# Optimization experiments

Hardware: AMD Instinct MI355X
Metric: run time of the kernel (lower is better)

The kernel has to match this reference:

```python
import jax, jax.numpy as jnp
import numpy as np

NUM_CLASSES = 6     # terrain classes 0..5
NUM_SUBJECTS = 16   # subject ids 0..15
MARGIN = 1.0
EPS = 1e-6          # torch pairwise_distance eps (added to the difference)


def setup_inputs() -> dict:
    key = jax.random.key(0)
    k1, k2, k3 = jax.random.split(key, 3)
    B, D = 131072, 256
    emb = jax.random.normal(k1, (B, D), dtype=jnp.float32)
    labels = jax.random.randint(k2, (B,), 0, NUM_CLASSES)
    sbj = jax.random.randint(k3, (B,), 0, NUM_SUBJECTS)
    return {"emb": emb, "labels": labels, "sbj": sbj}


def reference(emb, labels, sbj):
    """Within-subject hard-negative triplet loss.

    For every (subject s, class c) group with >=2 positives and >=1 negative
    (negatives = same subject, different class):
      anchor = first positive (in batch order), positive = second positive,
      negative = hardest (closest to anchor) same-subject other-class sample.
    Loss = mean over valid triplets of relu(d(a,p) - d(a,n) + margin), p=2.
    """
    B, D = emb.shape
    # flat grid of all (subject, class) pairs: P = NUM_SUBJECTS * NUM_CLASSES
    s_grid = jnp.repeat(jnp.arange(NUM_SUBJECTS), NUM_CLASSES)
    c_grid = jnp.tile(jnp.arange(NUM_CLASSES), NUM_SUBJECTS)

    def per_pair(s, c):
        m_pos = (sbj == s) & (labels == c)          # (B,)
        m_neg = (sbj == s) & (labels != c)          # (B,)
        cs = jnp.cumsum(m_pos)
        anchor_idx = jnp.argmax(m_pos & (cs == 1))  # first positive in batch order
        pos_idx = jnp.argmax(m_pos & (cs == 2))     # second positive
        valid = (jnp.sum(m_pos) >= 2) & (jnp.sum(m_neg) >= 1)
        return anchor_idx, pos_idx, m_neg, valid

    anchor_idx, pos_idx, m_neg, valid = jax.vmap(per_pair)(s_grid, c_grid)

    a = emb[anchor_idx]                              # (P, D)
    # squared L2 distance from each anchor to every sample (for mining only;
    # argmin of squared distance == argmin of distance, matching torch.cdist)
    d2 = (jnp.sum(a * a, axis=-1)[:, None]
          + jnp.sum(emb * emb, axis=-1)[None, :]
          - 2.0 * (a @ emb.T))                       # (P, B)
    d2 = jnp.where(m_neg, d2, jnp.inf)
    neg_idx = jnp.argmin(d2, axis=1)                 # (P,) hardest negative

    p = emb[pos_idx]                                 # (P, D)
    n = emb[neg_idx]                                 # (P, D)
    # torch TripletMarginLoss uses pairwise_distance: ||x1 - x2 + eps||_2
    d_ap = jnp.linalg.norm(a - p + EPS, axis=-1)
    d_an = jnp.linalg.norm(a - n + EPS, axis=-1)
    per_triplet = jnp.maximum(d_ap - d_an + MARGIN, 0.0)

    vf = valid.astype(emb.dtype)
    cnt = jnp.sum(vf)
    loss = jnp.sum(per_triplet * vf) / jnp.maximum(cnt, 1.0)
    return jnp.where(cnt > 0, loss, jnp.zeros((), emb.dtype))
```

## Files before the change

### kernel.cpp

```cpp
#include <hip/hip_runtime.h>

#define NUM_CLASSES 6
#define NUM_SUBJECTS 16
#define NUM_PAIRS (NUM_CLASSES * NUM_SUBJECTS)
#define MARGIN 1.0f
#define EPS 1e-6f
#define INF_I 0x7fffffff


__device__ __forceinline__ float wredsum(float v) {
#pragma unroll
    for (int m = 32; m >= 1; m >>= 1) v += __shfl_xor(v, m, 64);
    return v;
}

__device__ __forceinline__ unsigned int fkey(float f) {
    unsigned int b = __float_as_uint(f);
    return (b & 0x80000000u) ? ~b : (b | 0x80000000u);
}

__device__ __forceinline__ unsigned short f2bf(float f) {
    unsigned int u = __float_as_uint(f);
    unsigned int r = u + 0x7fffu + ((u >> 16) & 1u);
    return (unsigned short)(r >> 16);
}

__global__ void k_init(int* min1, int* min2, int* cntPos, int* cntSbj,
                       unsigned long long* best, float* a2) {
    int t = threadIdx.x;
    if (t < NUM_PAIRS) {
        min1[t] = INF_I;
        min2[t] = INF_I;
        cntPos[t] = 0;
        best[t] = ~0ull;
        a2[t] = 0.f;
    }
    if (t < NUM_SUBJECTS) cntSbj[t] = 0;
}

__global__ void k_stats(const int* __restrict__ labels, const int* __restrict__ sbj,
                        int* min1, int* min2, int* cntPos, int* cntSbj, int B) {
    __shared__ int l1[NUM_PAIRS], l2[NUM_PAIRS], lcp[NUM_PAIRS], lcs[NUM_SUBJECTS];
    for (int t = threadIdx.x; t < NUM_PAIRS; t += blockDim.x) { l1[t] = INF_I; l2[t] = INF_I; lcp[t] = 0; }
    if (threadIdx.x < NUM_SUBJECTS) lcs[threadIdx.x] = 0;
    __syncthreads();
    int i = blockIdx.x * blockDim.x + threadIdx.x;
    if (i < B) {
        int s = sbj[i], c = labels[i];
        int p = s * NUM_CLASSES + c;
        int o = atomicMin(&l1[p], i);
        atomicMin(&l2[p], max(o, i));
        atomicAdd(&lcp[p], 1);
        atomicAdd(&lcs[s], 1);
    }
    __syncthreads();
    for (int t = threadIdx.x; t < NUM_PAIRS; t += blockDim.x) {
        int m1 = l1[t];
        if (m1 != INF_I) {
            int o = atomicMin(&min1[t], m1);
            atomicMin(&min2[t], max(o, m1));
            if (l2[t] != INF_I) atomicMin(&min2[t], l2[t]);
            atomicAdd(&cntPos[t], lcp[t]);
        }
    }
    if (threadIdx.x < NUM_SUBJECTS && lcs[threadIdx.x]) atomicAdd(&cntSbj[threadIdx.x], lcs[threadIdx.x]);
}

__global__ void k_gather(const float4* __restrict__ emb4, const int* __restrict__ min1,
                         float4* anchors4, float* a2, int B) {
    int p = blockIdx.x;
    int lane = threadIdx.x;
    int idx = min1[p];
    if (idx < 0 || idx >= B) idx = 0;
    float4 v = emb4[(size_t)idx * 64 + lane];
    anchors4[(size_t)p * 64 + lane] = v;
    float t = v.x * v.x + v.y * v.y + v.z * v.z + v.w * v.w;
    t = wredsum(t);
    if (lane == 0) a2[p] = t;
}

__global__ __launch_bounds__(512, 2) void k_mine(const float4* __restrict__ emb4,
                                                 const int* __restrict__ labels,
                                                 const int* __restrict__ sbj,
                                                 const float4* __restrict__ anchors4,
                                                 const float* __restrict__ a2,
                                                 unsigned long long* gbest, int B) {
    __shared__ unsigned long long ancB64[NUM_SUBJECTS * 385];
    __shared__ float a2l[NUM_PAIRS];
    __shared__ unsigned long long lbest[NUM_PAIRS];

    for (int u = threadIdx.x; u < NUM_PAIRS * 64; u += blockDim.x) {
        int row = u >> 6;
        int grp = u & 63;
        float4 v = anchors4[u];
        unsigned int lo = (unsigned int)f2bf(v.x) | ((unsigned int)f2bf(v.y) << 16);
        unsigned int hi = (unsigned int)f2bf(v.z) | ((unsigned int)f2bf(v.w) << 16);
        int s = row / NUM_CLASSES, c = row - s * NUM_CLASSES;
        ancB64[s * 385 + c * 64 + grp] = (unsigned long long)lo | ((unsigned long long)hi << 32);
    }
    for (int t = threadIdx.x; t < NUM_PAIRS; t += blockDim.x) {
        a2l[t] = a2[t];
        lbest[t] = ~0ull;
    }
    __syncthreads();

    const int lane = threadIdx.x & 63;
    const int wv = (int)(threadIdx.x >> 6);
    const int wavesPerBlk = (int)(blockDim.x >> 6);
    const int waveGlob = (int)blockIdx.x * wavesPerBlk + wv;
    const int nwv = (int)gridDim.x * wavesPerBlk;
    const int nchunk = (B + 63) >> 6;

    for (int ch = waveGlob; ch < nchunk; ch += nwv) {
        int i = ch * 64 + lane;
        bool valid = i < B;
        int ic = valid ? i : (B - 1);
        int s = sbj[ic];
        int lbl = labels[ic];
        const float4* row = emb4 + (size_t)ic * 64;
        const unsigned long long* anc = ancB64 + s * 385;
        float e2 = 0.f, d0 = 0.f, d1 = 0.f, d2v = 0.f, d3 = 0.f, d4 = 0.f, d5 = 0.f;
#pragma unroll 4
        for (int k = 0; k < 64; ++k) {
            float4 v = row[k];
            e2 = fmaf(v.x, v.x, fmaf(v.y, v.y, fmaf(v.z, v.z, fmaf(v.w, v.w, e2))));
            unsigned long long A;
            unsigned int lo, hi;
            float a0, a1, a2f, a3;
#define DOT(C, ACC)                                                              \
            A = anc[(C) * 64 + k];                                               \
            lo = (unsigned int)A; hi = (unsigned int)(A >> 32);                  \
            a0 = __uint_as_float(lo << 16);                                      \
            a1 = __uint_as_float(lo & 0xffff0000u);                              \
            a2f = __uint_as_float(hi << 16);                                     \
            a3 = __uint_as_float(hi & 0xffff0000u);                              \
            ACC = fmaf(a0, v.x, fmaf(a1, v.y, fmaf(a2f, v.z, fmaf(a3, v.w, ACC))));
            DOT(0, d0) DOT(1, d1) DOT(2, d2v) DOT(3, d3) DOT(4, d4) DOT(5, d5)
#undef DOT
        }
        if (valid) {
            int pb = s * NUM_CLASSES;
            float dc[NUM_CLASSES] = {d0, d1, d2v, d3, d4, d5};
#pragma unroll
            for (int c = 0; c < NUM_CLASSES; ++c) {
                if (c != lbl) {
                    float dd = a2l[pb + c] + e2 - 2.f * dc[c];
                    unsigned long long pk =
                        ((unsigned long long)fkey(dd) << 32) | (unsigned int)i;
                    atomicMin(&lbest[pb + c], pk);
                }
            }
        }
    }
    __syncthreads();
    for (int t = threadIdx.x; t < NUM_PAIRS; t += blockDim.x) {
        unsigned long long v = lbest[t];
        if (v != ~0ull) {
            unsigned long long cur = gbest[t];
            if (v < cur) atomicMin(&gbest[t], v);
        }
    }
}

__global__ __launch_bounds__(1024) void k_finalize(const float4* __restrict__ emb4,
                                                   const int* __restrict__ min1,
                                                   const int* __restrict__ min2,
                                                   const int* __restrict__ cntPos,
                                                   const int* __restrict__ cntSbj,
                                                   const unsigned long long* __restrict__ best,
                                                   float* out, int B) {
    __shared__ float vals[NUM_PAIRS];
    __shared__ int vld[NUM_PAIRS];
    int wave = threadIdx.x >> 6;
    int lane = threadIdx.x & 63;
    for (int p = wave; p < NUM_PAIRS; p += (blockDim.x >> 6)) {
        int s = p / NUM_CLASSES;
        int ai = min1[p], pi = min2[p];
        int npos = cntPos[p];
        int nneg = cntSbj[s] - npos;
        unsigned long long bb = best[p];
        int ni = (int)(bb & 0xffffffffu);
        bool ok = (npos >= 2) && (nneg >= 1) && (bb != ~0ull);
        if (ai < 0 || ai >= B) ai = 0;
        if (pi < 0 || pi >= B) pi = 0;
        if (ni < 0 || ni >= B) ni = 0;
        float4 a = emb4[(size_t)ai * 64 + lane];
        float4 pp = emb4[(size_t)pi * 64 + lane];
        float4 nn = emb4[(size_t)ni * 64 + lane];
        float dap = 0.f, dan = 0.f, t;
        t = a.x - pp.x + EPS; dap += t * t;
        t = a.y - pp.y + EPS; dap += t * t;
        t = a.z - pp.z + EPS; dap += t * t;
        t = a.w - pp.w + EPS; dap += t * t;
        t = a.x - nn.x + EPS; dan += t * t;
        t = a.y - nn.y + EPS; dan += t * t;
        t = a.z - nn.z + EPS; dan += t * t;
        t = a.w - nn.w + EPS; dan += t * t;
        dap = wredsum(dap);
        dan = wredsum(dan);
        if (lane == 0) {
            float lv = sqrtf(dap) - sqrtf(dan) + MARGIN;
            vals[p] = ok ? fmaxf(lv, 0.f) : 0.f;
            vld[p] = ok ? 1 : 0;
        }
    }
    __syncthreads();
    if (threadIdx.x == 0) {
        float sum = 0.f;
        int cnt = 0;
        for (int p = 0; p < NUM_PAIRS; ++p) { sum += vals[p]; cnt += vld[p]; }
        out[0] = (cnt > 0) ? (sum / (float)cnt) : 0.f;
    }
}

extern "C" void kernel_launch(void* const* d_in, const int* in_sizes, int n_in,
                              void* d_out, int out_size, void* d_ws, size_t ws_size,
                              hipStream_t stream) {
    const float* emb = (const float*)d_in[0];
    const int* labels = (const int*)d_in[1];
    const int* sbj = (const int*)d_in[2];
    float* out = (float*)d_out;
    const int B = in_sizes[1];
    const float4* emb4 = (const float4*)emb;

    char* ws = (char*)d_ws;
    int* min1 = (int*)(ws + 0);
    int* min2 = (int*)(ws + 384);
    int* cntPos = (int*)(ws + 768);
    int* cntSbj = (int*)(ws + 1152);
    unsigned long long* best = (unsigned long long*)(ws + 1216);
    float* a2 = (float*)(ws + 1984);
    float4* anchors4 = (float4*)(ws + 2432);

    k_init<<<1, 128, 0, stream>>>(min1, min2, cntPos, cntSbj, best, a2);

    int blk = 256;
    int grd = (B + blk - 1) / blk;
    k_stats<<<grd, blk, 0, stream>>>(labels, sbj, min1, min2, cntPos, cntSbj, B);

    k_gather<<<NUM_PAIRS, 64, 0, stream>>>(emb4, min1, anchors4, a2, B);

    int nchunk = (B + 63) >> 6;
    int mblocks = (nchunk + 7) / 8;
    if (mblocks > 2048) mblocks = 2048;
    k_mine<<<mblocks, 512, 0, stream>>>(emb4, labels, sbj, anchors4, a2, best, B);

    k_finalize<<<1, 1024, 0, stream>>>(emb4, min1, min2, cntPos, cntSbj, best, out, B);
}
```

Baseline: 80.40 us.

## Use fp16 packed dot products and split each sample row across two lanes

Anchors are now stored as fp16 pairs instead of bf16, and embeddings are converted to fp16 so the distance dot products use v_dot2 (fdot2) instructions. Each sample is handled by two lanes that each take half of the 256 dimensions, with the partial sums combined by a shuffle, and the grid is sized to one sample per lane pair instead of a grid-stride loop. Launch bounds are raised to 4 blocks per CU. This cuts ALU work for the mining dot products and adds parallelism. The cost is fp16 range and precision limits on the values that choose the hardest negative.

```diff
diff --git a/kernel.cpp b/kernel.cpp
--- a/kernel.cpp
+++ b/kernel.cpp
@@ -7,6 +7,8 @@
 #define EPS 1e-6f
 #define INF_I 0x7fffffff
 
+typedef _Float16 h2_t __attribute__((ext_vector_type(2)));
+
 
 __device__ __forceinline__ float wredsum(float v) {
 #pragma unroll
@@ -19,10 +21,8 @@
     return (b & 0x80000000u) ? ~b : (b | 0x80000000u);
 }
 
-__device__ __forceinline__ unsigned short f2bf(float f) {
-    unsigned int u = __float_as_uint(f);
-    unsigned int r = u + 0x7fffu + ((u >> 16) & 1u);
-    return (unsigned short)(r >> 16);
+__device__ __forceinline__ h2_t pk16(float x, float y) {
+    return __builtin_bit_cast(h2_t, __builtin_amdgcn_cvt_pkrtz(x, y));
 }
 
 __global__ void k_init(int* min1, int* min2, int* cntPos, int* cntSbj,
@@ -79,24 +79,24 @@
     if (lane == 0) a2[p] = t;
 }
 
-__global__ __launch_bounds__(512, 2) void k_mine(const float4* __restrict__ emb4,
+__global__ __launch_bounds__(512, 4) void k_mine(const float4* __restrict__ emb4,
                                                  const int* __restrict__ labels,
                                                  const int* __restrict__ sbj,
                                                  const float4* __restrict__ anchors4,
                                                  const float* __restrict__ a2,
                                                  unsigned long long* gbest, int B) {
-    __shared__ unsigned long long ancB64[NUM_SUBJECTS * 385];
+    __shared__ unsigned long long ancB[NUM_SUBJECTS * 385];
     __shared__ float a2l[NUM_PAIRS];
     __shared__ unsigned long long lbest[NUM_PAIRS];
 
     for (int u = threadIdx.x; u < NUM_PAIRS * 64; u += blockDim.x) {
         int row = u >> 6;
-        int grp = u & 63;
+        int e = u & 63;
         float4 v = anchors4[u];
-        unsigned int lo = (unsigned int)f2bf(v.x) | ((unsigned int)f2bf(v.y) << 16);
-        unsigned int hi = (unsigned int)f2bf(v.z) | ((unsigned int)f2bf(v.w) << 16);
+        unsigned int lou = __builtin_bit_cast(unsigned int, pk16(v.x, v.y));
+        unsigned int hiu = __builtin_bit_cast(unsigned int, pk16(v.z, v.w));
         int s = row / NUM_CLASSES, c = row - s * NUM_CLASSES;
-        ancB64[s * 385 + c * 64 + grp] = (unsigned long long)lo | ((unsigned long long)hi << 32);
+        ancB[s * 385 + c * 64 + e] = (unsigned long long)lou | ((unsigned long long)hiu << 32);
     }
     for (int t = threadIdx.x; t < NUM_PAIRS; t += blockDim.x) {
         a2l[t] = a2[t];
@@ -105,50 +105,61 @@
     __syncthreads();
 
     const int lane = threadIdx.x & 63;
+    const int h = lane & 1;
     const int wv = (int)(threadIdx.x >> 6);
-    const int wavesPerBlk = (int)(blockDim.x >> 6);
-    const int waveGlob = (int)blockIdx.x * wavesPerBlk + wv;
-    const int nwv = (int)gridDim.x * wavesPerBlk;
-    const int nchunk = (B + 63) >> 6;
-
-    for (int ch = waveGlob; ch < nchunk; ch += nwv) {
-        int i = ch * 64 + lane;
-        bool valid = i < B;
-        int ic = valid ? i : (B - 1);
-        int s = sbj[ic];
-        int lbl = labels[ic];
-        const float4* row = emb4 + (size_t)ic * 64;
-        const unsigned long long* anc = ancB64 + s * 385;
-        float e2 = 0.f, d0 = 0.f, d1 = 0.f, d2v = 0.f, d3 = 0.f, d4 = 0.f, d5 = 0.f;
+    const int sample = (int)blockIdx.x * 256 + wv * 32 + (lane >> 1);
+    const bool valid = sample < B;
+    const int ic = valid ? sample : (B - 1);
+    const int s = sbj[ic];
+    const int lbl = labels[ic];
+    const float4* row = emb4 + (size_t)ic * 64 + h * 32;
+    const unsigned long long* anc = ancB + s * 385 + h * 32;
+
+    float e2 = 0.f, d0 = 0.f, d1 = 0.f, d2v = 0.f, d3 = 0.f, d4 = 0.f, d5 = 0.f;
 #pragma unroll 4
-        for (int k = 0; k < 64; ++k) {
-            float4 v = row[k];
-            e2 = fmaf(v.x, v.x, fmaf(v.y, v.y, fmaf(v.z, v.z, fmaf(v.w, v.w, e2))));
-            unsigned long long A;
-            unsigned int lo, hi;
-            float a0, a1, a2f, a3;
+    for (int k = 0; k < 32; ++k) {
+        float4 v = row[k];
+        e2 = fmaf(v.x, v.x, fmaf(v.y, v.y, fmaf(v.z, v.z, fmaf(v.w, v.w, e2))));
+        h2_t vlo = pk16(v.x, v.y);
+        h2_t vhi = pk16(v.z, v.w);
+        unsigned long long A;
+        h2_t alo, ahi;
+#if __has_builtin(__builtin_amdgcn_fdot2)
 #define DOT(C, ACC)                                                              \
-            A = anc[(C) * 64 + k];                                               \
-            lo = (unsigned int)A; hi = (unsigned int)(A >> 32);                  \
-            a0 = __uint_as_float(lo << 16);                                      \
-            a1 = __uint_as_float(lo & 0xffff0000u);                              \
-            a2f = __uint_as_float(hi << 16);                                     \
-            a3 = __uint_as_float(hi & 0xffff0000u);                              \
-            ACC = fmaf(a0, v.x, fmaf(a1, v.y, fmaf(a2f, v.z, fmaf(a3, v.w, ACC))));
-            DOT(0, d0) DOT(1, d1) DOT(2, d2v) DOT(3, d3) DOT(4, d4) DOT(5, d5)
+        A = anc[(C) * 64 + k];                                                   \
+        alo = __builtin_bit_cast(h2_t, (unsigned int)A);                         \
+        ahi = __builtin_bit_cast(h2_t, (unsigned int)(A >> 32));                 \
+        ACC = __builtin_amdgcn_fdot2(alo, vlo,                                   \
+              __builtin_amdgcn_fdot2(ahi, vhi, ACC, false), false);
+#else
+#define DOT(C, ACC)                                                              \
+        A = anc[(C) * 64 + k];                                                   \
+        alo = __builtin_bit_cast(h2_t, (unsigned int)A);                         \
+        ahi = __builtin_bit_cast(h2_t, (unsigned int)(A >> 32));                 \
+        ACC = fmaf((float)alo.x, v.x, fmaf((float)alo.y, v.y,                    \
+              fmaf((float)ahi.x, v.z, fmaf((float)ahi.y, v.w, ACC))));
+#endif
+        DOT(0, d0) DOT(1, d1) DOT(2, d2v) DOT(3, d3) DOT(4, d4) DOT(5, d5)
 #undef DOT
-        }
-        if (valid) {
-            int pb = s * NUM_CLASSES;
-            float dc[NUM_CLASSES] = {d0, d1, d2v, d3, d4, d5};
+    }
+    e2  += __shfl_xor(e2, 1, 64);
+    d0  += __shfl_xor(d0, 1, 64);
+    d1  += __shfl_xor(d1, 1, 64);
+    d2v += __shfl_xor(d2v, 1, 64);
+    d3  += __shfl_xor(d3, 1, 64);
+    d4  += __shfl_xor(d4, 1, 64);
+    d5  += __shfl_xor(d5, 1, 64);
+
+    if (valid && h == 0) {
+        int pb = s * NUM_CLASSES;
+        float dc[NUM_CLASSES] = {d0, d1, d2v, d3, d4, d5};
 #pragma unroll
-            for (int c = 0; c < NUM_CLASSES; ++c) {
-                if (c != lbl) {
-                    float dd = a2l[pb + c] + e2 - 2.f * dc[c];
-                    unsigned long long pk =
-                        ((unsigned long long)fkey(dd) << 32) | (unsigned int)i;
-                    atomicMin(&lbest[pb + c], pk);
-                }
+        for (int c = 0; c < NUM_CLASSES; ++c) {
+            if (c != lbl) {
+                float dd = a2l[pb + c] + e2 - 2.f * dc[c];
+                unsigned long long pk =
+                    ((unsigned long long)fkey(dd) << 32) | (unsigned int)sample;
+                atomicMin(&lbest[pb + c], pk);
             }
         }
     }
@@ -240,9 +251,7 @@
 
     k_gather<<<NUM_PAIRS, 64, 0, stream>>>(emb4, min1, anchors4, a2, B);
 
-    int nchunk = (B + 63) >> 6;
-    int mblocks = (nchunk + 7) / 8;
-    if (mblocks > 2048) mblocks = 2048;
+    int mblocks = (B + 255) / 256;
     k_mine<<<mblocks, 512, 0, stream>>>(emb4, labels, sbj, anchors4, a2, best, B);
 
     k_finalize<<<1, 1024, 0, stream>>>(emb4, min1, min2, cntPos, cntSbj, best, out, B);
```

Measured after the change: 81.11 us. No clear change (+0.9%).
